# Optimization experiments

Hardware: AMD Instinct MI355X
Metric: run time of the kernel (lower is better)

Reference implementation:

```python
import jax, jax.numpy as jnp
import numpy as np

N_NODES = 80000
N_EDGES = 1280000
IN_CH = 128
HID = 64
N_GRAPHS = 64
DROPOUT_P = 0.3


def setup_inputs() -> dict:
    key = jax.random.key(0)
    ks = jax.random.split(key, 12)
    x = jax.random.normal(ks[0], (N_NODES, IN_CH), dtype=jnp.float32)
    edge_index = jax.random.randint(ks[1], (2, N_EDGES), 0, N_NODES, dtype=jnp.int64 if jax.config.read('jax_enable_x64') else jnp.int32)
    batch = jnp.sort(jax.random.randint(ks[2], (N_NODES,), 0, N_GRAPHS))
    def lin(k, fan_in, fan_out):
        lim = 1.0 / np.sqrt(fan_in)
        kw, kb = jax.random.split(k)
        W = jax.random.uniform(kw, (fan_in, fan_out), minval=-lim, maxval=lim, dtype=jnp.float32)
        b = jax.random.uniform(kb, (fan_out,), minval=-lim, maxval=lim, dtype=jnp.float32)
        return W, b
    W1, b1 = lin(ks[3], IN_CH, HID)
    W2, b2 = lin(ks[4], HID, HID)
    W3, b3 = lin(ks[5], HID, HID)
    Wm1, bm1 = lin(ks[6], HID, HID)
    Wm2, bm2 = lin(ks[7], HID, 1)
    return {"x": x, "edge_index": edge_index, "batch": batch,
            "W1": W1, "b1": b1, "W2": W2, "b2": b2, "W3": W3, "b3": b3,
            "Wm1": Wm1, "bm1": bm1, "Wm2": Wm2, "bm2": bm2}


def _gcn_conv(x, W, b, src, dst, deg_inv_sqrt):
    # PyG GCNConv: h = X W; add self-loops; norm_e = d^-1/2[src] * d^-1/2[dst]
    h = x @ W  # [N, F]
    norm = deg_inv_sqrt[src] * deg_inv_sqrt[dst]  # [E]
    agg = jax.ops.segment_sum(h[src] * norm[:, None], dst, num_segments=x.shape[0])
    agg = agg + h * (deg_inv_sqrt * deg_inv_sqrt)[:, None]  # self-loop term d^-1
    return agg + b


def _dropout(x, key, p):
    keep = jax.random.bernoulli(key, 1.0 - p, x.shape)
    return jnp.where(keep, x / (1.0 - p), 0.0)


def reference(x, edge_index, batch, W1, b1, W2, b2, W3, b3, Wm1, bm1, Wm2, bm2):
    src, dst = edge_index[0], edge_index[1]
    N = x.shape[0]
    # in-degree on dst, +1 for self-loop (PyG default normalization)
    deg = jax.ops.segment_sum(jnp.ones_like(dst, dtype=x.dtype), dst, num_segments=N) + 1.0
    deg_inv_sqrt = jax.lax.rsqrt(deg)

    dk = jax.random.split(jax.random.key(42), 4)
    h = _dropout(jax.nn.relu(_gcn_conv(x, W1, b1, src, dst, deg_inv_sqrt)), dk[0], DROPOUT_P)
    h = _dropout(jax.nn.relu(_gcn_conv(h, W2, b2, src, dst, deg_inv_sqrt)), dk[1], DROPOUT_P)
    h = _dropout(jax.nn.relu(_gcn_conv(h, W3, b3, src, dst, deg_inv_sqrt)), dk[2], DROPOUT_P)

    # global mean pool per graph
    sums = jax.ops.segment_sum(h, batch, num_segments=N_GRAPHS)
    counts = jax.ops.segment_sum(jnp.ones((N,), dtype=h.dtype), batch, num_segments=N_GRAPHS)
    pooled = sums / jnp.maximum(counts, 1.0)[:, None]  # [G, HID]

    # MLP head: Linear -> ReLU -> Dropout -> Linear
    m = jax.nn.relu(pooled @ Wm1 + bm1)
    m = _dropout(m, dk[3], DROPOUT_P)
    return m @ Wm2 + bm2  # [G, 1]
```

## Files before the change

### kernel.cpp

```cpp
#include <hip/hip_runtime.h>
#include <hip/hip_fp8.h>
#include <stdint.h>

#define HID 64
#define INCH 128
#define NGRAPH 64
#define KEEPP 0.7f
#define CAP 64
#define CAPSH 6

typedef __attribute__((ext_vector_type(8))) short short8;
typedef __attribute__((ext_vector_type(4))) float floatx4;

__device__ __forceinline__ uint8_t f2e4(float f) {
  __hip_fp8_e4m3 t(f);
  return (uint8_t)t.__x;
}
__device__ __forceinline__ float e42f(uint8_t b) {
  __hip_fp8_e4m3 t;
  t.__x = (__hip_fp8_storage_t)b;
  return (float)t;
}

__host__ __device__ inline void tf2x32(uint32_t k0, uint32_t k1,
                                       uint32_t& x0, uint32_t& x1) {
  const uint32_t ks2 = k0 ^ k1 ^ 0x1BD11BDAu;
#define ROTL32(v, d) (((v) << (d)) | ((v) >> (32 - (d))))
#define TF_RND(r) { x0 += x1; x1 = ROTL32(x1, r); x1 ^= x0; }
  x0 += k0; x1 += k1;
  TF_RND(13) TF_RND(15) TF_RND(26) TF_RND(6)
  x0 += k1;  x1 += ks2 + 1u;
  TF_RND(17) TF_RND(29) TF_RND(16) TF_RND(24)
  x0 += ks2; x1 += k0 + 2u;
  TF_RND(13) TF_RND(15) TF_RND(26) TF_RND(6)
  x0 += k0;  x1 += k1 + 3u;
  TF_RND(17) TF_RND(29) TF_RND(16) TF_RND(24)
  x0 += k1;  x1 += ks2 + 4u;
  TF_RND(13) TF_RND(15) TF_RND(26) TF_RND(6)
  x0 += ks2; x1 += k0 + 5u;
#undef TF_RND
#undef ROTL32
}

__device__ __forceinline__ bool keep_mask(uint32_t k0, uint32_t k1, uint32_t idx) {
  uint32_t x0 = 0u, x1 = idx;
  tf2x32(k0, k1, x0, x1);
  uint32_t bits = x0 ^ x1;
  float u = __uint_as_float((bits >> 9) | 0x3f800000u) - 1.0f;
  return u < KEEPP;
}

__device__ __forceinline__ void wsplit_one(const float* __restrict__ W,
                                           short8* __restrict__ Wh,
                                           short8* __restrict__ Wl, int i) {
  int lane = i & 63, f = i >> 6;
  int kc = f >> 2, ct = f & 3;
  int kbase = kc * 32 + ((lane >> 4) << 3);
  int n = ct * 16 + (lane & 15);
  short8 h, l;
#pragma unroll
  for (int j = 0; j < 8; ++j) {
    float w = W[(size_t)(kbase + j) * HID + n];
    uint32_t u = __float_as_uint(w);
    h[j] = (short)(u >> 16);
    float r = w - __uint_as_float(u & 0xFFFF0000u);
    l[j] = (short)(__float_as_uint(r) >> 16);
  }
  Wh[i] = h;
  Wl[i] = l;
}

__global__ __launch_bounds__(1024) void k_prep(
    const float* __restrict__ W1, short8* __restrict__ Wh1, short8* __restrict__ Wl1,
    const float* __restrict__ W2, short8* __restrict__ Wh2, short8* __restrict__ Wl2,
    const float* __restrict__ W3, short8* __restrict__ Wh3, short8* __restrict__ Wl3,
    int* __restrict__ counts, float* __restrict__ sums, float* __restrict__ cnts,
    int N) {
  const int b = blockIdx.x;
  const int tid = threadIdx.x;
  if (b == 0) {
    wsplit_one(W1, Wh1, Wl1, tid);
  } else if (b == 1) {
    if (tid < 512) wsplit_one(W2, Wh2, Wl2, tid);
  } else if (b == 2) {
    if (tid < 512) wsplit_one(W3, Wh3, Wl3, tid);
  } else {
    for (int i = tid; i < N; i += 1024) counts[i] = 0;
    for (int i = tid; i < NGRAPH * HID; i += 1024) sums[i] = 0.0f;
    if (tid < NGRAPH) cnts[tid] = 0.0f;
  }
}

__global__ __launch_bounds__(256) void k_build(const int* __restrict__ src,
                                               const int* __restrict__ dst,
                                               int* __restrict__ counts,
                                               int* __restrict__ cap, int E) {
  int e = blockIdx.x * 256 + threadIdx.x;
  if (e < E) {
    int s = src[e], d = dst[e];
    int r = atomicAdd(&counts[d], 1);
    if (r < CAP) cap[(d << CAPSH) + r] = s;
  }
}

template <int K>
__global__ __launch_bounds__(256) void k_mgemm_s(const float* __restrict__ A,
                                                 const short8* __restrict__ Wh,
                                                 const short8* __restrict__ Wl,
                                                 uint8_t* __restrict__ C,
                                                 const int* __restrict__ counts,
                                                 int N) {
  constexpr int KC = K / 32;
  const int lane = threadIdx.x & 63;
  const int wv = threadIdx.x >> 6;
  const int m = lane & 15;
  const int q = lane >> 4;
  const int row0 = (int)blockIdx.x * 64 + wv * 16;
  if (row0 >= N) return;
  const int arow = min(row0 + m, N - 1);
  const float* __restrict__ ap = A + (size_t)arow * K + (q << 3);

  floatx4 acc[4];
#pragma unroll
  for (int ct = 0; ct < 4; ++ct) acc[ct] = (floatx4){0.f, 0.f, 0.f, 0.f};

#pragma unroll
  for (int kc = 0; kc < KC; ++kc) {
    const floatx4* apv = (const floatx4*)(ap + kc * 32);
    floatx4 x0 = apv[0];
    floatx4 x1 = apv[1];
    short8 ah, al;
#pragma unroll
    for (int j = 0; j < 4; ++j) {
      uint32_t u = __float_as_uint(x0[j]);
      ah[j] = (short)(u >> 16);
      float r = x0[j] - __uint_as_float(u & 0xFFFF0000u);
      al[j] = (short)(__float_as_uint(r) >> 16);
    }
#pragma unroll
    for (int j = 0; j < 4; ++j) {
      uint32_t u = __float_as_uint(x1[j]);
      ah[4 + j] = (short)(u >> 16);
      float r = x1[j] - __uint_as_float(u & 0xFFFF0000u);
      al[4 + j] = (short)(__float_as_uint(r) >> 16);
    }
#pragma unroll
    for (int ct = 0; ct < 4; ++ct) {
      short8 bh = Wh[(kc * 4 + ct) * 64 + lane];
      short8 bl = Wl[(kc * 4 + ct) * 64 + lane];
      acc[ct] = __builtin_amdgcn_mfma_f32_16x16x32_bf16(ah, bh, acc[ct], 0, 0, 0);
      acc[ct] = __builtin_amdgcn_mfma_f32_16x16x32_bf16(ah, bl, acc[ct], 0, 0, 0);
      acc[ct] = __builtin_amdgcn_mfma_f32_16x16x32_bf16(al, bh, acc[ct], 0, 0, 0);
    }
  }

  float dv[4];
#pragma unroll
  for (int r = 0; r < 4; ++r) {
    int gr = min(row0 + (q << 2) + r, N - 1);
    dv[r] = rsqrtf((float)counts[gr] + 1.0f);
  }

  uint8_t* __restrict__ cp = C + (size_t)row0 * HID;
#pragma unroll
  for (int ct = 0; ct < 4; ++ct)
#pragma unroll
    for (int r = 0; r < 4; ++r) {
      int rr = (q << 2) + r;
      if (row0 + rr < N) cp[(size_t)rr * HID + ct * 16 + m] = f2e4(acc[ct][r] * dv[r]);
    }
}

__global__ __launch_bounds__(256) void k_gather_s(const uint8_t* __restrict__ tmp,
                                                  const int* __restrict__ counts,
                                                  const int* __restrict__ cap,
                                                  const float* __restrict__ bias,
                                                  float* __restrict__ outh, int N,
                                                  uint32_t k0, uint32_t k1) {
  const int node = blockIdx.x * 4 + (threadIdx.x >> 6);
  const int lane = threadIdx.x & 63;
  if (node >= N) return;
  const int degn = __builtin_amdgcn_readfirstlane(counts[node]);
  const int deg = min(degn, CAP);
  const int base = node << CAPSH;
  float acc0 = 0.0f, acc1 = 0.0f, acc2 = 0.0f, acc3 = 0.0f;
  int j = 0;
  for (; j + 7 < deg; j += 8) {
    int4 e0 = *(const int4*)&cap[base + j];
    int4 e1 = *(const int4*)&cap[base + j + 4];
    float v0 = e42f(tmp[(size_t)e0.x * HID + lane]);
    float v1 = e42f(tmp[(size_t)e0.y * HID + lane]);
    float v2 = e42f(tmp[(size_t)e0.z * HID + lane]);
    float v3 = e42f(tmp[(size_t)e0.w * HID + lane]);
    float v4 = e42f(tmp[(size_t)e1.x * HID + lane]);
    float v5 = e42f(tmp[(size_t)e1.y * HID + lane]);
    float v6 = e42f(tmp[(size_t)e1.z * HID + lane]);
    float v7 = e42f(tmp[(size_t)e1.w * HID + lane]);
    acc0 += v0; acc1 += v1; acc2 += v2; acc3 += v3;
    acc0 += v4; acc1 += v5; acc2 += v6; acc3 += v7;
  }
  for (; j + 1 < deg; j += 2) {
    int2 p = *(const int2*)&cap[base + j];
    acc0 += e42f(tmp[(size_t)p.x * HID + lane]);
    acc1 += e42f(tmp[(size_t)p.y * HID + lane]);
  }
  if (j < deg) {
    int s = cap[base + j];
    acc2 += e42f(tmp[(size_t)s * HID + lane]);
  }
  float acc = (acc0 + acc1) + (acc2 + acc3);
  const float dn = rsqrtf((float)degn + 1.0f);
  const int idx = node * HID + lane;
  float v = dn * (acc + e42f(tmp[idx])) + bias[lane];
  v = fmaxf(v, 0.0f);
  v = keep_mask(k0, k1, (uint32_t)idx) ? v / KEEPP : 0.0f;
  outh[idx] = v;
}

__global__ __launch_bounds__(256) void k_pool(const float* __restrict__ h,
                                              const int* __restrict__ batch,
                                              float* __restrict__ sums,
                                              float* __restrict__ cnts, int N) {
  __shared__ float ls[NGRAPH * HID];
  __shared__ float lc[NGRAPH];
  for (int i = threadIdx.x; i < NGRAPH * HID; i += 256) ls[i] = 0.0f;
  if (threadIdx.x < NGRAPH) lc[threadIdx.x] = 0.0f;
  __syncthreads();
  const int lane = threadIdx.x & 63;
  const int wave = threadIdx.x >> 6;
  int per = (N + gridDim.x - 1) / gridDim.x;
  int beg = blockIdx.x * per;
  int end = min(N, beg + per);
  for (int i = beg + wave; i < end; i += 4) {
    int g = batch[i];
    atomicAdd(&ls[g * HID + lane], h[(size_t)i * HID + lane]);
    if (lane == 0) atomicAdd(&lc[g], 1.0f);
  }
  __syncthreads();
  for (int i = threadIdx.x; i < NGRAPH * HID; i += 256)
    if (ls[i] != 0.0f) atomicAdd(&sums[i], ls[i]);
  if (threadIdx.x < NGRAPH && lc[threadIdx.x] != 0.0f)
    atomicAdd(&cnts[threadIdx.x], lc[threadIdx.x]);
}

__global__ __launch_bounds__(256) void k_head(const float* __restrict__ sums,
                                              const float* __restrict__ cnts,
                                              const float* __restrict__ Wm1,
                                              const float* __restrict__ bm1,
                                              const float* __restrict__ Wm2,
                                              const float* __restrict__ bm2,
                                              float* __restrict__ out,
                                              uint32_t k0, uint32_t k1) {
  __shared__ float pooled[NGRAPH * HID];
  __shared__ float m[NGRAPH * HID];
  for (int i = threadIdx.x; i < NGRAPH * HID; i += 256) {
    int g = i >> 6;
    pooled[i] = sums[i] / fmaxf(cnts[g], 1.0f);
  }
  __syncthreads();
  for (int i = threadIdx.x; i < NGRAPH * HID; i += 256) {
    int g = i >> 6, j = i & 63;
    float acc = bm1[j];
#pragma unroll 8
    for (int k = 0; k < HID; ++k)
      acc = fmaf(pooled[g * HID + k], Wm1[k * HID + j], acc);
    acc = fmaxf(acc, 0.0f);
    m[i] = keep_mask(k0, k1, (uint32_t)i) ? acc / KEEPP : 0.0f;
  }
  __syncthreads();
  if (threadIdx.x < NGRAPH) {
    int g = threadIdx.x;
    float acc = bm2[0];
#pragma unroll 8
    for (int j = 0; j < HID; ++j)
      acc = fmaf(m[g * HID + j], Wm2[j], acc);
    out[g] = acc;
  }
}

extern "C" void kernel_launch(void* const* d_in, const int* in_sizes, int n_in,
                              void* d_out, int out_size, void* d_ws, size_t ws_size,
                              hipStream_t stream) {
  const float* x     = (const float*)d_in[0];
  const int*   ei    = (const int*)d_in[1];
  const int*   batch = (const int*)d_in[2];
  const float* W1 = (const float*)d_in[3];
  const float* b1 = (const float*)d_in[4];
  const float* W2 = (const float*)d_in[5];
  const float* b2 = (const float*)d_in[6];
  const float* W3 = (const float*)d_in[7];
  const float* b3 = (const float*)d_in[8];
  const float* Wm1 = (const float*)d_in[9];
  const float* bm1 = (const float*)d_in[10];
  const float* Wm2 = (const float*)d_in[11];
  const float* bm2 = (const float*)d_in[12];
  float* out = (float*)d_out;

  const int N = in_sizes[0] / INCH;
  const int E = in_sizes[1] / 2;
  const int* src = ei;
  const int* dst = ei + E;

  char* ws = (char*)d_ws;
  size_t off = 0;
  uint8_t* B0 = (uint8_t*)(ws + off); off += (size_t)N * HID;
  off = (off + 15) & ~(size_t)15;
  float* B1     = (float*)(ws + off); off += (size_t)N * HID * 4;
  int*   counts = (int*)  (ws + off); off += (size_t)N * 4;
  int*   cap    = (int*)  (ws + off); off += (size_t)N * CAP * 4;
  float* sums   = (float*)(ws + off); off += NGRAPH * HID * 4;
  float* cnts   = (float*)(ws + off); off += NGRAPH * 4;
  off = (off + 15) & ~(size_t)15;
  short8* Wh1 = (short8*)(ws + off); off += 1024 * 16;
  short8* Wl1 = (short8*)(ws + off); off += 1024 * 16;
  short8* Wh2 = (short8*)(ws + off); off += 512 * 16;
  short8* Wl2 = (short8*)(ws + off); off += 512 * 16;
  short8* Wh3 = (short8*)(ws + off); off += 512 * 16;
  short8* Wl3 = (short8*)(ws + off); off += 512 * 16;

  uint32_t dk[4][2];
  for (uint32_t i = 0; i < 4; ++i) {
    uint32_t a = 0u, b = i;
    tf2x32(0u, 42u, a, b);
    dk[i][0] = a; dk[i][1] = b;
  }

  const int build_grid = (E + 255) / 256;
  const int mg_grid    = (N + 63) / 64;
  const int gath_grid  = (N + 3) / 4;

  k_prep<<<4, 1024, 0, stream>>>(W1, Wh1, Wl1, W2, Wh2, Wl2, W3, Wh3, Wl3,
                                 counts, sums, cnts, N);
  k_build<<<build_grid, 256, 0, stream>>>(src, dst, counts, cap, E);

  k_mgemm_s<INCH><<<mg_grid, 256, 0, stream>>>(x, Wh1, Wl1, B0, counts, N);
  k_gather_s<<<gath_grid, 256, 0, stream>>>(B0, counts, cap, b1,
                                            B1, N, dk[0][0], dk[0][1]);
  k_mgemm_s<HID><<<mg_grid, 256, 0, stream>>>(B1, Wh2, Wl2, B0, counts, N);
  k_gather_s<<<gath_grid, 256, 0, stream>>>(B0, counts, cap, b2,
                                            B1, N, dk[1][0], dk[1][1]);
  k_mgemm_s<HID><<<mg_grid, 256, 0, stream>>>(B1, Wh3, Wl3, B0, counts, N);
  k_gather_s<<<gath_grid, 256, 0, stream>>>(B0, counts, cap, b3,
                                            B1, N, dk[2][0], dk[2][1]);

  k_pool<<<256, 256, 0, stream>>>(B1, batch, sums, cnts, N);
  k_head<<<1, 256, 0, stream>>>(sums, cnts, Wm1, bm1, Wm2, bm2, out,
                                dk[3][0], dk[3][1]);
  (void)n_in; (void)out_size; (void)ws_size;
}
```

Baseline: 407.9 us.

## Split degree counting from CSR fill and co-schedule fill with first GEMM

Degree counting moves into the prep kernel as extra blocks, so the first GEMM can use final degrees, while the adjacency fill (using a separate cursor array) runs in the same launch as the first GEMM with blocks interleaved. Per-graph node counts are computed once in prep from the sorted batch array instead of by atomics in the pool kernel. The gather kernel also hoists its self-term and bias loads ahead of the neighbour loop. This removes a kernel boundary and overlaps the atomic-heavy fill with MFMA work, at the cost of an extra memset, an extra pass over dst, and a 1024-thread serial scan per chunk for graph counts.

Result: slower. 463.4 us (+13.6%).

```diff
diff --git a/kernel.cpp b/kernel.cpp
--- a/kernel.cpp
+++ b/kernel.cpp
@@ -75,7 +75,7 @@
     const float* __restrict__ W2, short8* __restrict__ Wh2, short8* __restrict__ Wl2,
     const float* __restrict__ W3, short8* __restrict__ Wh3, short8* __restrict__ Wl3,
     int* __restrict__ counts, float* __restrict__ sums, float* __restrict__ cnts,
-    int N) {
+    const int* __restrict__ batch, const int* __restrict__ dst, int N, int E) {
   const int b = blockIdx.x;
   const int tid = threadIdx.x;
   if (b == 0) {
@@ -84,23 +84,122 @@
     if (tid < 512) wsplit_one(W2, Wh2, Wl2, tid);
   } else if (b == 2) {
     if (tid < 512) wsplit_one(W3, Wh3, Wl3, tid);
+  } else if (b == 3) {
+    __shared__ int hist[NGRAPH];
+    if (tid < NGRAPH) hist[tid] = 0;
+    __syncthreads();
+    for (int i = tid; i < NGRAPH * HID; i += 1024) sums[i] = 0.0f;
+    int chunk = (N + 1023) / 1024;
+    int beg = tid * chunk, end = min(N, beg + chunk);
+    int gprev = -1, run = 0;
+    for (int i = beg; i < end; ++i) {
+      int g = batch[i];
+      if (g != gprev) {
+        if (run > 0) atomicAdd(&hist[gprev], run);
+        gprev = g; run = 0;
+      }
+      ++run;
+    }
+    if (run > 0 && gprev >= 0) atomicAdd(&hist[gprev], run);
+    __syncthreads();
+    if (tid < NGRAPH) cnts[tid] = (float)hist[tid];
   } else {
-    for (int i = tid; i < N; i += 1024) counts[i] = 0;
-    for (int i = tid; i < NGRAPH * HID; i += 1024) sums[i] = 0.0f;
-    if (tid < NGRAPH) cnts[tid] = 0.0f;
-  }
-}
-
-__global__ __launch_bounds__(256) void k_build(const int* __restrict__ src,
-                                               const int* __restrict__ dst,
-                                               int* __restrict__ counts,
-                                               int* __restrict__ cap, int E) {
-  int e = blockIdx.x * 256 + threadIdx.x;
-  if (e < E) {
-    int s = src[e], d = dst[e];
-    int r = atomicAdd(&counts[d], 1);
-    if (r < CAP) cap[(d << CAPSH) + r] = s;
-  }
+    int e = (b - 4) * 1024 + tid;
+    if (e < E) atomicAdd(&counts[dst[e]], 1);
+  }
+}
+
+template <int K>
+__device__ __forceinline__ void mgemm_s_tile(const float* __restrict__ A,
+                                             const short8* __restrict__ Wh,
+                                             const short8* __restrict__ Wl,
+                                             uint8_t* __restrict__ C,
+                                             const int* __restrict__ counts,
+                                             int N, int tile) {
+  constexpr int KC = K / 32;
+  const int lane = threadIdx.x & 63;
+  const int wv = threadIdx.x >> 6;
+  const int m = lane & 15;
+  const int q = lane >> 4;
+  const int row0 = tile * 64 + wv * 16;
+  if (row0 >= N) return;
+  const int arow = min(row0 + m, N - 1);
+  const float* __restrict__ ap = A + (size_t)arow * K + (q << 3);
+
+  floatx4 acc[4];
+#pragma unroll
+  for (int ct = 0; ct < 4; ++ct) acc[ct] = (floatx4){0.f, 0.f, 0.f, 0.f};
+
+#pragma unroll
+  for (int kc = 0; kc < KC; ++kc) {
+    const floatx4* apv = (const floatx4*)(ap + kc * 32);
+    floatx4 x0 = apv[0];
+    floatx4 x1 = apv[1];
+    short8 ah, al;
+#pragma unroll
+    for (int j = 0; j < 4; ++j) {
+      uint32_t u = __float_as_uint(x0[j]);
+      ah[j] = (short)(u >> 16);
+      float r = x0[j] - __uint_as_float(u & 0xFFFF0000u);
+      al[j] = (short)(__float_as_uint(r) >> 16);
+    }
+#pragma unroll
+    for (int j = 0; j < 4; ++j) {
+      uint32_t u = __float_as_uint(x1[j]);
+      ah[4 + j] = (short)(u >> 16);
+      float r = x1[j] - __uint_as_float(u & 0xFFFF0000u);
+      al[4 + j] = (short)(__float_as_uint(r) >> 16);
+    }
+#pragma unroll
+    for (int ct = 0; ct < 4; ++ct) {
+      short8 bh = Wh[(kc * 4 + ct) * 64 + lane];
+      short8 bl = Wl[(kc * 4 + ct) * 64 + lane];
+      acc[ct] = __builtin_amdgcn_mfma_f32_16x16x32_bf16(ah, bh, acc[ct], 0, 0, 0);
+      acc[ct] = __builtin_amdgcn_mfma_f32_16x16x32_bf16(ah, bl, acc[ct], 0, 0, 0);
+      acc[ct] = __builtin_amdgcn_mfma_f32_16x16x32_bf16(al, bh, acc[ct], 0, 0, 0);
+    }
+  }
+
+  float dv[4];
+#pragma unroll
+  for (int r = 0; r < 4; ++r) {
+    int gr = min(row0 + (q << 2) + r, N - 1);
+    dv[r] = rsqrtf((float)counts[gr] + 1.0f);
+  }
+
+  uint8_t* __restrict__ cp = C + (size_t)row0 * HID;
+#pragma unroll
+  for (int ct = 0; ct < 4; ++ct)
+#pragma unroll
+    for (int r = 0; r < 4; ++r) {
+      int rr = (q << 2) + r;
+      if (row0 + rr < N) cp[(size_t)rr * HID + ct * 16 + m] = f2e4(acc[ct][r] * dv[r]);
+    }
+}
+
+template <int K>
+__global__ __launch_bounds__(256) void k_build_gemm(
+    const float* __restrict__ A, const short8* __restrict__ Wh,
+    const short8* __restrict__ Wl, uint8_t* __restrict__ C,
+    const int* __restrict__ counts, int N,
+    const int* __restrict__ src, const int* __restrict__ dst,
+    int* __restrict__ cursor, int* __restrict__ cap,
+    int E, int build_blocks, int gemm_blocks) {
+  const long T = (long)build_blocks + gemm_blocks;
+  const long b = (long)blockIdx.x;
+  const long gb = (b * gemm_blocks) / T;
+  const bool is_g = (((b + 1) * gemm_blocks) / T) != gb;
+  if (!is_g) {
+    int bb = (int)(b - gb);
+    int e = bb * 256 + (int)threadIdx.x;
+    if (e < E) {
+      int s = src[e], d = dst[e];
+      int r = atomicAdd(&cursor[d], 1);
+      if (r < CAP) cap[(d << CAPSH) + r] = s;
+    }
+    return;
+  }
+  mgemm_s_tile<K>(A, Wh, Wl, C, counts, N, (int)gb);
 }
 
 template <int K>
@@ -110,65 +209,7 @@
                                                  uint8_t* __restrict__ C,
                                                  const int* __restrict__ counts,
                                                  int N) {
-  constexpr int KC = K / 32;
-  const int lane = threadIdx.x & 63;
-  const int wv = threadIdx.x >> 6;
-  const int m = lane & 15;
-  const int q = lane >> 4;
-  const int row0 = (int)blockIdx.x * 64 + wv * 16;
-  if (row0 >= N) return;
-  const int arow = min(row0 + m, N - 1);
-  const float* __restrict__ ap = A + (size_t)arow * K + (q << 3);
-
-  floatx4 acc[4];
-#pragma unroll
-  for (int ct = 0; ct < 4; ++ct) acc[ct] = (floatx4){0.f, 0.f, 0.f, 0.f};
-
-#pragma unroll
-  for (int kc = 0; kc < KC; ++kc) {
-    const floatx4* apv = (const floatx4*)(ap + kc * 32);
-    floatx4 x0 = apv[0];
-    floatx4 x1 = apv[1];
-    short8 ah, al;
-#pragma unroll
-    for (int j = 0; j < 4; ++j) {
-      uint32_t u = __float_as_uint(x0[j]);
-      ah[j] = (short)(u >> 16);
-      float r = x0[j] - __uint_as_float(u & 0xFFFF0000u);
-      al[j] = (short)(__float_as_uint(r) >> 16);
-    }
-#pragma unroll
-    for (int j = 0; j < 4; ++j) {
-      uint32_t u = __float_as_uint(x1[j]);
-      ah[4 + j] = (short)(u >> 16);
-      float r = x1[j] - __uint_as_float(u & 0xFFFF0000u);
-      al[4 + j] = (short)(__float_as_uint(r) >> 16);
-    }
-#pragma unroll
-    for (int ct = 0; ct < 4; ++ct) {
-      short8 bh = Wh[(kc * 4 + ct) * 64 + lane];
-      short8 bl = Wl[(kc * 4 + ct) * 64 + lane];
-      acc[ct] = __builtin_amdgcn_mfma_f32_16x16x32_bf16(ah, bh, acc[ct], 0, 0, 0);
-      acc[ct] = __builtin_amdgcn_mfma_f32_16x16x32_bf16(ah, bl, acc[ct], 0, 0, 0);
-      acc[ct] = __builtin_amdgcn_mfma_f32_16x16x32_bf16(al, bh, acc[ct], 0, 0, 0);
-    }
-  }
-
-  float dv[4];
-#pragma unroll
-  for (int r = 0; r < 4; ++r) {
-    int gr = min(row0 + (q << 2) + r, N - 1);
-    dv[r] = rsqrtf((float)counts[gr] + 1.0f);
-  }
-
-  uint8_t* __restrict__ cp = C + (size_t)row0 * HID;
-#pragma unroll
-  for (int ct = 0; ct < 4; ++ct)
-#pragma unroll
-    for (int r = 0; r < 4; ++r) {
-      int rr = (q << 2) + r;
-      if (row0 + rr < N) cp[(size_t)rr * HID + ct * 16 + m] = f2e4(acc[ct][r] * dv[r]);
-    }
+  mgemm_s_tile<K>(A, Wh, Wl, C, counts, N, (int)blockIdx.x);
 }
 
 __global__ __launch_bounds__(256) void k_gather_s(const uint8_t* __restrict__ tmp,
@@ -183,6 +224,9 @@
   const int degn = __builtin_amdgcn_readfirstlane(counts[node]);
   const int deg = min(degn, CAP);
   const int base = node << CAPSH;
+  const int idx = node * HID + lane;
+  const float selfv = e42f(tmp[idx]);
+  const float blane = bias[lane];
   float acc0 = 0.0f, acc1 = 0.0f, acc2 = 0.0f, acc3 = 0.0f;
   int j = 0;
   for (; j + 7 < deg; j += 8) {
@@ -210,8 +254,7 @@
   }
   float acc = (acc0 + acc1) + (acc2 + acc3);
   const float dn = rsqrtf((float)degn + 1.0f);
-  const int idx = node * HID + lane;
-  float v = dn * (acc + e42f(tmp[idx])) + bias[lane];
+  float v = dn * (acc + selfv) + blane;
   v = fmaxf(v, 0.0f);
   v = keep_mask(k0, k1, (uint32_t)idx) ? v / KEEPP : 0.0f;
   outh[idx] = v;
@@ -239,8 +282,7 @@
   __syncthreads();
   for (int i = threadIdx.x; i < NGRAPH * HID; i += 256)
     if (ls[i] != 0.0f) atomicAdd(&sums[i], ls[i]);
-  if (threadIdx.x < NGRAPH && lc[threadIdx.x] != 0.0f)
-    atomicAdd(&cnts[threadIdx.x], lc[threadIdx.x]);
+  (void)cnts;
 }
 
 __global__ __launch_bounds__(256) void k_head(const float* __restrict__ sums,
@@ -307,6 +349,7 @@
   off = (off + 15) & ~(size_t)15;
   float* B1     = (float*)(ws + off); off += (size_t)N * HID * 4;
   int*   counts = (int*)  (ws + off); off += (size_t)N * 4;
+  int*   cursor = (int*)  (ws + off); off += (size_t)N * 4;
   int*   cap    = (int*)  (ws + off); off += (size_t)N * CAP * 4;
   float* sums   = (float*)(ws + off); off += NGRAPH * HID * 4;
   float* cnts   = (float*)(ws + off); off += NGRAPH * 4;
@@ -325,15 +368,18 @@
     dk[i][0] = a; dk[i][1] = b;
   }
 
-  const int build_grid = (E + 255) / 256;
-  const int mg_grid    = (N + 63) / 64;
-  const int gath_grid  = (N + 3) / 4;
-
-  k_prep<<<4, 1024, 0, stream>>>(W1, Wh1, Wl1, W2, Wh2, Wl2, W3, Wh3, Wl3,
-                                 counts, sums, cnts, N);
-  k_build<<<build_grid, 256, 0, stream>>>(src, dst, counts, cap, E);
-
-  k_mgemm_s<INCH><<<mg_grid, 256, 0, stream>>>(x, Wh1, Wl1, B0, counts, N);
+  const int count_blocks = (E + 1023) / 1024;
+  const int build_grid   = (E + 255) / 256;
+  const int mg_grid      = (N + 63) / 64;
+  const int gath_grid    = (N + 3) / 4;
+
+  hipMemsetAsync(counts, 0, (size_t)N * 8, stream);
+  k_prep<<<4 + count_blocks, 1024, 0, stream>>>(
+      W1, Wh1, Wl1, W2, Wh2, Wl2, W3, Wh3, Wl3,
+      counts, sums, cnts, batch, dst, N, E);
+
+  k_build_gemm<INCH><<<build_grid + mg_grid, 256, 0, stream>>>(
+      x, Wh1, Wl1, B0, counts, N, src, dst, cursor, cap, E, build_grid, mg_grid);
   k_gather_s<<<gath_grid, 256, 0, stream>>>(B0, counts, cap, b1,
                                             B1, N, dk[0][0], dk[0][1]);
   k_mgemm_s<HID><<<mg_grid, 256, 0, stream>>>(B1, Wh2, Wl2, B0, counts, N);
```
